# Kernel optimization log

Hardware: AMD Instinct MI355X
Metric: run time of the kernel (lower is better)

Reference implementation:

```python
import jax, jax.numpy as jnp
import numpy as np


def setup_inputs() -> dict:
    key = jax.random.key(0)
    k1, k2, k3 = jax.random.split(key, 3)
    B, S, D = 2, 2048, 1024
    N_COMPRESS, RANK = 64, 64
    x = jax.random.normal(k1, (B, S, D), dtype=jnp.float32)
    router_w = jax.random.normal(k2, (N_COMPRESS, D), dtype=jnp.float32) * (1.0 / np.sqrt(D))
    # compress neurons (orthogonal-init in torch; gaussian scaled is fine for a numeric baseline)
    neurons = jax.random.normal(k3, (N_COMPRESS, D, RANK), dtype=jnp.float32) * (1.0 / np.sqrt(D))
    return {"x": x, "router_w": router_w, "neurons": neurons}


TOP_K = 2


def reference(x, router_w, neurons):
    # x: [B,S,D], router_w: [N,D], neurons: [N,D,R]
    B, S, D = x.shape
    R = neurons.shape[-1]
    scores = jnp.einsum('bsd,nd->bsn', x, router_w)            # [B,S,N]
    topk_scores, topk_idx = jax.lax.top_k(scores, TOP_K)       # [B,S,K]
    topk_weights = jax.nn.softmax(topk_scores, axis=-1)        # [B,S,K]
    output = jnp.zeros((B, S, R), dtype=x.dtype)
    for i in range(TOP_K):  # small fixed loop, mirrors original slot-wise combine
        idx = topk_idx[:, :, i]                                # [B,S]
        sel = neurons[idx]                                     # [B,S,D,R] gather
        proj = jnp.einsum('bsd,bsdr->bsr', x, sel)             # per-token matvec
        output = output + topk_weights[:, :, i:i + 1] * proj
    return output, topk_idx, topk_weights
```

## Files before the change

kernel.cpp:

```cpp
#include <hip/hip_runtime.h>
#include <hip/hip_bf16.h>


typedef unsigned short u16;
typedef unsigned int u32;
typedef __attribute__((ext_vector_type(8))) short short8;
typedef __attribute__((ext_vector_type(4))) float f32x4;

__device__ __forceinline__ float bf2f(u16 u) {
    u32 v = ((u32)u) << 16; float f; __builtin_memcpy(&f, &v, 4); return f;
}
__device__ __forceinline__ u16 f2bf(float f) {
    u32 u; __builtin_memcpy(&u, &f, 4);
    u32 r = u + 0x7fff + ((u >> 16) & 1);
    return (u16)(r >> 16);
}
__device__ __forceinline__ u32 pack2(float a, float b) {
    return ((u32)f2bf(b) << 16) | (u32)f2bf(a);
}

#define T_TOKENS 4096
#define DDIM 1024
#define NEXP 64
#define RDIM 64
#define LCAP 1024
#define OUT_IDX_OFF 262144
#define OUT_W_OFF 270336

struct LdBF {
    const u16* p;
    __device__ __forceinline__ float4 ld4(size_t i) const {
        ushort4 v = *(const ushort4*)(p + i);
        return make_float4(bf2f(v.x), bf2f(v.y), bf2f(v.z), bf2f(v.w));
    }
    __device__ __forceinline__ float ld1(size_t i) const { return bf2f(p[i]); }
};
struct LdF32 {
    const float* p;
    __device__ __forceinline__ float4 ld4(size_t i) const { return *(const float4*)(p + i); }
    __device__ __forceinline__ float ld1(size_t i) const { return p[i]; }
};

__device__ __forceinline__ int detect_f32(const u16* x, int* lds_cnt) {
    if (threadIdx.x == 0) *lds_cnt = 0;
    __syncthreads();
    if (threadIdx.x < 256) {
        unsigned e = (x[threadIdx.x] >> 7) & 0xFF;
        if (e >= 0x68 && e <= 0x88) atomicAdd(lds_cnt, 1);
    }
    __syncthreads();
    int f = (*lds_cnt < 200) ? 1 : 0;
    __syncthreads();
    return f;
}

template <class LD>
__device__ __forceinline__ void score_body(LD xld, LD rwld,
                                           float* xs , float* wt ,
                                           float* sc ,
                                           float* out, float* wsW,
                                           int* wsCnt, int* wsList) {
    const int tid = threadIdx.x;
    const size_t t0 = (size_t)blockIdx.x * 16;
    const int wv = tid >> 6;
    const int lane = tid & 63;
    const int tg = lane & 1;
    const int eg = (lane >> 1) & 7;
    const int kql = (lane >> 4) & 3;
    const int dd = 4 * kql + 16 * wv;

    {
        float4 z = make_float4(0.f, 0.f, 0.f, 0.f);
        ((float4*)out)[(size_t)blockIdx.x * 256 + tid] = z;
    }

    const int sm = tid >> 4;
    const int sd4 = (tid & 15) * 4;

    float acc[8][8];
#pragma unroll
    for (int mi = 0; mi < 8; ++mi)
#pragma unroll
        for (int ei = 0; ei < 8; ++ei) acc[mi][ei] = 0.f;

    float4 px = xld.ld4((t0 + sm) * DDIM + sd4);
    float4 pw[4];
#pragma unroll
    for (int h = 0; h < 4; ++h) {
        int i4 = tid + h * 256;
        pw[h] = rwld.ld4((size_t)(i4 >> 4) * DDIM + (i4 & 15) * 4);
    }

    for (int kc = 0; kc < 16; ++kc) {
        if (kc > 0) __syncthreads();
        *(float4*)&xs[sm * 68 + sd4] = px;
#pragma unroll
        for (int h = 0; h < 4; ++h) {
            int i4 = tid + h * 256;
            *(float4*)&wt[(i4 >> 4) * 68 + (i4 & 15) * 4] = pw[h];
        }
        __syncthreads();

        if (kc < 15) {
            px = xld.ld4((t0 + sm) * DDIM + (kc + 1) * 64 + sd4);
#pragma unroll
            for (int h = 0; h < 4; ++h) {
                int i4 = tid + h * 256;
                pw[h] = rwld.ld4((size_t)(i4 >> 4) * DDIM + (kc + 1) * 64 + (i4 & 15) * 4);
            }
        }

        float4 xv[8], wv4[8];
#pragma unroll
        for (int mi = 0; mi < 8; ++mi)
            xv[mi] = *(const float4*)&xs[(tg + 2 * mi) * 68 + dd];
#pragma unroll
        for (int ei = 0; ei < 8; ++ei)
            wv4[ei] = *(const float4*)&wt[(eg + 8 * ei) * 68 + dd];
#pragma unroll
        for (int mi = 0; mi < 8; ++mi)
#pragma unroll
            for (int ei = 0; ei < 8; ++ei)
                acc[mi][ei] += xv[mi].x * wv4[ei].x + xv[mi].y * wv4[ei].y +
                               xv[mi].z * wv4[ei].z + xv[mi].w * wv4[ei].w;
    }

#pragma unroll
    for (int mi = 0; mi < 8; ++mi)
#pragma unroll
        for (int ei = 0; ei < 8; ++ei) {
            float v = acc[mi][ei];
            v += __shfl_xor(v, 16, 64);
            v += __shfl_xor(v, 32, 64);
            acc[mi][ei] = v;
        }
    __syncthreads();

    for (int w = 0; w < 4; ++w) {
        if (wv == w && kql == 0) {
#pragma unroll
            for (int mi = 0; mi < 8; ++mi)
#pragma unroll
                for (int ei = 0; ei < 8; ++ei) {
                    int idx = (tg + 2 * mi) * 65 + eg + 8 * ei;
                    sc[idx] = (w == 0) ? acc[mi][ei] : sc[idx] + acc[mi][ei];
                }
        }
        __syncthreads();
    }

    if (tid < 16) {
        const float* s = &sc[tid * 65];
        float best = -1e30f, secv = -1e30f;
        int bi = 0, si = 0;
        for (int j = 0; j < NEXP; ++j) {
            float v = s[j];
            if (v > best) { secv = best; si = bi; best = v; bi = j; }
            else if (v > secv) { secv = v; si = j; }
        }
        float w0 = 1.0f / (1.0f + expf(secv - best));
        float w1 = 1.0f - w0;
        size_t t = t0 + tid;
        out[OUT_IDX_OFF + t * 2 + 0] = (float)bi;
        out[OUT_IDX_OFF + t * 2 + 1] = (float)si;
        out[OUT_W_OFF + t * 2 + 0] = w0;
        out[OUT_W_OFF + t * 2 + 1] = w1;
        wsW[t * 2 + 0] = w0;
        wsW[t * 2 + 1] = w1;
        int p0 = atomicAdd(&wsCnt[bi], 1);
        if (p0 < LCAP) wsList[bi * LCAP + p0] = (int)(t * 2 + 0);
        int p1 = atomicAdd(&wsCnt[si], 1);
        if (p1 < LCAP) wsList[si * LCAP + p1] = (int)(t * 2 + 1);
    }
}

__global__ __launch_bounds__(256, 1) void score_topk(const void* x, const void* rw,
                                                     float* out, float* wsW,
                                                     int* wsCnt, int* wsList) {
    __shared__ float xs[16 * 68];
    __shared__ float wt[64 * 68];
    __shared__ float sc[16 * 65];
    __shared__ int dc;
    int f = detect_f32((const u16*)x, &dc);
    if (f)
        score_body(LdF32{(const float*)x}, LdF32{(const float*)rw}, xs, wt, sc, out, wsW, wsCnt, wsList);
    else
        score_body(LdBF{(const u16*)x}, LdBF{(const u16*)rw}, xs, wt, sc, out, wsW, wsCnt, wsList);
}

template <class LD>
__device__ __forceinline__ void egemm_body(LD xld, LD nld,
                                           const int* wsCnt, const int* wsList,
                                           const float* wsW, float* out,
                                           u16* Ab , u16* Bb ,
                                           int* entL ) {
    const int tid = threadIdx.x;
    const int e = blockIdx.x & 63;
    const int ti = blockIdx.x >> 6;
    const int cntE = min(wsCnt[e], LCAP);
    const int base = ti * 16;
    if (base >= cntE) return;
    const int valid = min(16, cntE - base);
    const int wv = tid >> 6;
    const int lane = tid & 63;
    const int l15 = lane & 15, quad = lane >> 4;
    const size_t nbase = (size_t)e * (DDIM * RDIM);

    if (tid < 16)
        entL[tid] = wsList[e * LCAP + base + min(tid, valid - 1)];
    __syncthreads();

    f32x4 acc = {0.f, 0.f, 0.f, 0.f};

    for (int kc = 0; kc < 8; ++kc) {
        const int k0c = kc * 128;
        if (kc > 0) __syncthreads();
#pragma unroll
        for (int h = 0; h < 16; ++h) {
            int p = tid + h * 256;
            int r = p & 63, kp = p >> 6;
            float g0 = nld.ld1(nbase + (size_t)(k0c + 2 * kp) * RDIM + r);
            float g1 = nld.ld1(nbase + (size_t)(k0c + 2 * kp + 1) * RDIM + r);
            ((u32*)Bb)[r * 68 + kp] = pack2(g0, g1);
        }
#pragma unroll
        for (int h = 0; h < 4; ++h) {
            int p = tid + h * 256;
            int row = p >> 6, kp = p & 63;
            size_t tt = (size_t)(entL[row] >> 1);
            float g0 = xld.ld1(tt * DDIM + k0c + 2 * kp);
            float g1 = xld.ld1(tt * DDIM + k0c + 2 * kp + 1);
            ((u32*)Ab)[row * 68 + kp] = pack2(g0, g1);
        }
        __syncthreads();

#pragma unroll
        for (int ko = 0; ko < 4; ++ko) {
            int kofs = ko * 32 + quad * 8;
            short8 bfr = *(const short8*)&Bb[(16 * wv + l15) * 136 + kofs];
            short8 af = *(const short8*)&Ab[l15 * 136 + kofs];
            acc = __builtin_amdgcn_mfma_f32_16x16x32_bf16(af, bfr, acc, 0, 0, 0);
        }
    }

#pragma unroll
    for (int reg = 0; reg < 4; ++reg) {
        int m = quad * 4 + reg;
        if (m < valid) {
            int t2 = entL[m];
            atomicAdd(&out[(size_t)(t2 >> 1) * RDIM + 16 * wv + l15], wsW[t2] * acc[reg]);
        }
    }
}

__global__ __launch_bounds__(256) void expert_gemm(const void* x, const void* neurons,
                                                   const int* wsCnt, const int* wsList,
                                                   const float* wsW, float* out) {
    __shared__ u16 Ab[16 * 136];
    __shared__ u16 Bb[64 * 136];
    __shared__ int entL[16];
    __shared__ int dc;
    int f = detect_f32((const u16*)x, &dc);
    if (f)
        egemm_body(LdF32{(const float*)x}, LdF32{(const float*)neurons}, wsCnt, wsList, wsW, out, Ab, Bb, entL);
    else
        egemm_body(LdBF{(const u16*)x}, LdBF{(const u16*)neurons}, wsCnt, wsList, wsW, out, Ab, Bb, entL);
}

extern "C" void kernel_launch(void* const* d_in, const int* in_sizes, int n_in,
                              void* d_out, int out_size, void* d_ws, size_t ws_size,
                              hipStream_t stream) {
    const void* x = d_in[0];
    const void* rw = d_in[1];
    const void* neurons = d_in[2];
    float* out = (float*)d_out;

    char* wsc = (char*)d_ws;
    float* wsW = (float*)wsc;
    int* wsCnt = (int*)(wsc + 32 * 1024);
    int* wsList = (int*)((char*)wsCnt + 256);

    hipMemsetAsync(wsCnt, 0, 256, stream);
    score_topk<<<256, 256, 0, stream>>>(x, rw, out, wsW, wsCnt, wsList);
    expert_gemm<<<1024, 256, 0, stream>>>(x, neurons, wsCnt, wsList, wsW, out);
}
```

Baseline: 128.3 us.

## Double-buffer score tiles and vectorize expert GEMM operand loads

The score_topk kernel now keeps two shared-memory buffers for the x and router tiles. The next chunk is written into the alternate buffer after compute, which removes one barrier per iteration. The expert GEMM kernel now loads neuron and token rows with float4 loads instead of scalar loads, which cuts global load instruction count. The cost is doubled LDS use in the score kernel and different LDS write patterns that may add bank conflicts.

```diff
diff --git a/kernel.cpp b/kernel.cpp
--- a/kernel.cpp
+++ b/kernel.cpp
@@ -83,24 +83,20 @@
 #pragma unroll
         for (int ei = 0; ei < 8; ++ei) acc[mi][ei] = 0.f;
 
-    float4 px = xld.ld4((t0 + sm) * DDIM + sd4);
-    float4 pw[4];
-#pragma unroll
-    for (int h = 0; h < 4; ++h) {
-        int i4 = tid + h * 256;
-        pw[h] = rwld.ld4((size_t)(i4 >> 4) * DDIM + (i4 & 15) * 4);
-    }
-
-    for (int kc = 0; kc < 16; ++kc) {
-        if (kc > 0) __syncthreads();
+    {
+        float4 px = xld.ld4((t0 + sm) * DDIM + sd4);
         *(float4*)&xs[sm * 68 + sd4] = px;
 #pragma unroll
         for (int h = 0; h < 4; ++h) {
             int i4 = tid + h * 256;
-            *(float4*)&wt[(i4 >> 4) * 68 + (i4 & 15) * 4] = pw[h];
-        }
-        __syncthreads();
-
+            float4 pw = rwld.ld4((size_t)(i4 >> 4) * DDIM + (i4 & 15) * 4);
+            *(float4*)&wt[(i4 >> 4) * 68 + (i4 & 15) * 4] = pw;
+        }
+    }
+    __syncthreads();
+
+    for (int kc = 0; kc < 16; ++kc) {
+        float4 px; float4 pw[4];
         if (kc < 15) {
             px = xld.ld4((t0 + sm) * DDIM + (kc + 1) * 64 + sd4);
 #pragma unroll
@@ -110,19 +106,33 @@
             }
         }
 
+        const float* xsb = xs + (kc & 1) * (16 * 68);
+        const float* wtb = wt + (kc & 1) * (64 * 68);
         float4 xv[8], wv4[8];
 #pragma unroll
         for (int mi = 0; mi < 8; ++mi)
-            xv[mi] = *(const float4*)&xs[(tg + 2 * mi) * 68 + dd];
+            xv[mi] = *(const float4*)&xsb[(tg + 2 * mi) * 68 + dd];
 #pragma unroll
         for (int ei = 0; ei < 8; ++ei)
-            wv4[ei] = *(const float4*)&wt[(eg + 8 * ei) * 68 + dd];
+            wv4[ei] = *(const float4*)&wtb[(eg + 8 * ei) * 68 + dd];
 #pragma unroll
         for (int mi = 0; mi < 8; ++mi)
 #pragma unroll
             for (int ei = 0; ei < 8; ++ei)
                 acc[mi][ei] += xv[mi].x * wv4[ei].x + xv[mi].y * wv4[ei].y +
                                xv[mi].z * wv4[ei].z + xv[mi].w * wv4[ei].w;
+
+        if (kc < 15) {
+            float* xsn = xs + ((kc + 1) & 1) * (16 * 68);
+            float* wtn = wt + ((kc + 1) & 1) * (64 * 68);
+            *(float4*)&xsn[sm * 68 + sd4] = px;
+#pragma unroll
+            for (int h = 0; h < 4; ++h) {
+                int i4 = tid + h * 256;
+                *(float4*)&wtn[(i4 >> 4) * 68 + (i4 & 15) * 4] = pw[h];
+            }
+            __syncthreads();
+        }
     }
 
 #pragma unroll
@@ -177,8 +187,8 @@
 __global__ __launch_bounds__(256, 1) void score_topk(const void* x, const void* rw,
                                                      float* out, float* wsW,
                                                      int* wsCnt, int* wsList) {
-    __shared__ float xs[16 * 68];
-    __shared__ float wt[64 * 68];
+    __shared__ float xs[2 * 16 * 68];
+    __shared__ float wt[2 * 64 * 68];
     __shared__ float sc[16 * 65];
     __shared__ int dc;
     int f = detect_f32((const u16*)x, &dc);
@@ -210,27 +220,35 @@
         entL[tid] = wsList[e * LCAP + base + min(tid, valid - 1)];
     __syncthreads();
 
+    const int rowA = tid & 15;
+    const int kq0 = tid >> 4;
+    const size_t ttA = (size_t)(entL[rowA] >> 1) * DDIM;
+
     f32x4 acc = {0.f, 0.f, 0.f, 0.f};
 
     for (int kc = 0; kc < 8; ++kc) {
         const int k0c = kc * 128;
         if (kc > 0) __syncthreads();
 #pragma unroll
-        for (int h = 0; h < 16; ++h) {
-            int p = tid + h * 256;
-            int r = p & 63, kp = p >> 6;
-            float g0 = nld.ld1(nbase + (size_t)(k0c + 2 * kp) * RDIM + r);
-            float g1 = nld.ld1(nbase + (size_t)(k0c + 2 * kp + 1) * RDIM + r);
-            ((u32*)Bb)[r * 68 + kp] = pack2(g0, g1);
-        }
-#pragma unroll
         for (int h = 0; h < 4; ++h) {
-            int p = tid + h * 256;
-            int row = p >> 6, kp = p & 63;
-            size_t tt = (size_t)(entL[row] >> 1);
-            float g0 = xld.ld1(tt * DDIM + k0c + 2 * kp);
-            float g1 = xld.ld1(tt * DDIM + k0c + 2 * kp + 1);
-            ((u32*)Ab)[row * 68 + kp] = pack2(g0, g1);
+            int u = tid + h * 256;
+            int rq = u & 15, kp = u >> 4;
+            float4 g0 = nld.ld4(nbase + (size_t)(k0c + 2 * kp) * RDIM + 4 * rq);
+            float4 g1 = nld.ld4(nbase + (size_t)(k0c + 2 * kp + 1) * RDIM + 4 * rq);
+            u32* bw = (u32*)Bb;
+            bw[(4 * rq + 0) * 68 + kp] = pack2(g0.x, g1.x);
+            bw[(4 * rq + 1) * 68 + kp] = pack2(g0.y, g1.y);
+            bw[(4 * rq + 2) * 68 + kp] = pack2(g0.z, g1.z);
+            bw[(4 * rq + 3) * 68 + kp] = pack2(g0.w, g1.w);
+        }
+        {
+            float4 ga0 = xld.ld4(ttA + k0c + 4 * kq0);
+            float4 ga1 = xld.ld4(ttA + k0c + 4 * (kq0 + 16));
+            u32* aw = (u32*)Ab;
+            aw[rowA * 68 + 2 * kq0 + 0]  = pack2(ga0.x, ga0.y);
+            aw[rowA * 68 + 2 * kq0 + 1]  = pack2(ga0.z, ga0.w);
+            aw[rowA * 68 + 2 * kq0 + 32] = pack2(ga1.x, ga1.y);
+            aw[rowA * 68 + 2 * kq0 + 33] = pack2(ga1.z, ga1.w);
         }
         __syncthreads();
 
```

Measured after the change: 151.3 us. 18.0% more time.
